# Kernel tuning notes

Hardware: AMD Instinct MI355X
Metric: run time of the kernel (lower is better)

## Reference

```python
import jax, jax.numpy as jnp
import numpy as np

N = 50000      # nodes
E = 800000     # edges per etype
IN, HID, OUT = 128, 128, 64
NH = 4         # heads in layerMH
NE = 2         # interaction edge types
NEG = 0.2      # GATConv leaky_relu negative slope


def _gat(x, src, dst, W, al, ar, b, heads, fdim):
    """DGL GATConv (residual=False, activation=None, bias=True).
    x: (N, in); W: (in, heads*fdim); al/ar: (heads, fdim); b: (heads*fdim,)
    Returns (N, heads, fdim)."""
    n = x.shape[0]
    z = (x @ W).reshape(n, heads, fdim)              # (N,H,F)
    el = jnp.sum(z * al, axis=-1)                    # (N,H)
    er = jnp.sum(z * ar, axis=-1)                    # (N,H)
    e = jax.nn.leaky_relu(el[src] + er[dst], NEG)    # (E,H)
    # edge softmax over incoming edges of each dst node
    m = jax.ops.segment_max(e, dst, num_segments=n)
    m = jnp.where(jnp.isfinite(m), m, 0.0)           # zero in-degree safety
    ex = jnp.exp(e - m[dst])
    den = jax.ops.segment_sum(ex, dst, num_segments=n)
    alpha = ex / jnp.maximum(den[dst], 1e-9)         # (E,H)
    out = jax.ops.segment_sum(alpha[:, :, None] * z[src], dst, num_segments=n)
    return out + b.reshape(1, heads, fdim)


def setup_inputs() -> dict:
    key = jax.random.key(0)
    ks = jax.random.split(key, 19)
    x = jax.random.normal(ks[0], (N, IN), jnp.float32)
    src0 = jax.random.randint(ks[1], (E,), 0, N, jnp.int32)
    dst0 = jax.random.randint(ks[2], (E,), 0, N, jnp.int32)
    src1 = jax.random.randint(ks[3], (E,), 0, N, jnp.int32)
    dst1 = jax.random.randint(ks[4], (E,), 0, N, jnp.int32)
    # per-etype GAT params (stacked over the NE edge types)
    W1 = jax.random.normal(ks[5], (NE, IN, HID), jnp.float32) / np.sqrt(IN)
    a_l1 = jax.random.normal(ks[6], (NE, 1, HID), jnp.float32) * 0.1
    a_r1 = jax.random.normal(ks[7], (NE, 1, HID), jnp.float32) * 0.1
    b1 = jnp.zeros((NE, HID), jnp.float32)
    W2 = jax.random.normal(ks[8], (NE, HID, OUT), jnp.float32) / np.sqrt(HID)
    a_l2 = jax.random.normal(ks[9], (NE, 1, OUT), jnp.float32) * 0.1
    a_r2 = jax.random.normal(ks[10], (NE, 1, OUT), jnp.float32) * 0.1
    b2 = jnp.zeros((NE, OUT), jnp.float32)
    Wm = jax.random.normal(ks[11], (NE, OUT, NH * OUT), jnp.float32) / np.sqrt(OUT)
    a_lm = jax.random.normal(ks[12], (NE, NH, OUT), jnp.float32) * 0.1
    a_rm = jax.random.normal(ks[13], (NE, NH, OUT), jnp.float32) * 0.1
    bm = jnp.zeros((NE, NH * OUT), jnp.float32)
    fc_w = jax.random.normal(ks[14], (NE, NE), jnp.float32) * (np.sqrt(2.0) / np.sqrt(NE))
    return dict(x=x, src0=src0, dst0=dst0, src1=src1, dst1=dst1,
                W1=W1, a_l1=a_l1, a_r1=a_r1, b1=b1,
                W2=W2, a_l2=a_l2, a_r2=a_r2, b2=b2,
                Wm=Wm, a_lm=a_lm, a_rm=a_rm, bm=bm, fc_w=fc_w)


def reference(x, src0, dst0, src1, dst1, W1, a_l1, a_r1, b1,
              W2, a_l2, a_r2, b2, Wm, a_lm, a_rm, bm, fc_w):
    srcs, dsts = (src0, src1), (dst0, dst1)
    # layer1: HeteroGraphConv mean over edge types, single head -> (N, HID)
    h1 = jnp.mean(jnp.stack([
        _gat(x, srcs[i], dsts[i], W1[i], a_l1[i], a_r1[i], b1[i], 1, HID)[:, 0, :]
        for i in range(NE)]), axis=0)
    # layer2: agg_func = fc over stacked etype axis, then mean -> (N, OUT)
    h2s = jnp.stack([
        _gat(h1, srcs[i], dsts[i], W2[i], a_l2[i], a_r2[i], b2[i], 1, OUT)[:, 0, :]
        for i in range(NE)], axis=-1)                       # (N, OUT, NE)
    h2 = jnp.mean(jnp.einsum('noe,fe->nof', h2s, fc_w), axis=-1)
    # multi-head layer: mean over edge types -> (N, NH, OUT)
    hm = jnp.mean(jnp.stack([
        _gat(h2, srcs[i], dsts[i], Wm[i], a_lm[i], a_rm[i], bm[i], NH, OUT)
        for i in range(NE)]), axis=0)
    # per-head mean-centering over nodes (vectorized over heads)
    return hm - jnp.mean(hm, axis=0, keepdims=True)
```

## Files before the change

### kernel.cpp

```cpp
#include <hip/hip_runtime.h>

#define NN 50000
#define EE 800000

using short8v = __attribute__((ext_vector_type(8))) short;
using f32x4 = __attribute__((ext_vector_type(4))) float;

__device__ inline unsigned int bf_pack(float lo, float hi) {
  unsigned int a = __float_as_uint(lo);
  a += 0x7FFFu + ((a >> 16) & 1u);
  unsigned int b = __float_as_uint(hi);
  b += 0x7FFFu + ((b >> 16) & 1u);
  return (a >> 16) | ((b >> 16) << 16);
}
__device__ inline void bf_dec8(uint4 v, float* f) {
  f[0] = __uint_as_float(v.x << 16); f[1] = __uint_as_float(v.x & 0xFFFF0000u);
  f[2] = __uint_as_float(v.y << 16); f[3] = __uint_as_float(v.y & 0xFFFF0000u);
  f[4] = __uint_as_float(v.z << 16); f[5] = __uint_as_float(v.z & 0xFFFF0000u);
  f[6] = __uint_as_float(v.w << 16); f[7] = __uint_as_float(v.w & 0xFFFF0000u);
}
__device__ inline float lrelu(float v) { return v >= 0.f ? v : 0.2f * v; }

__device__ inline void split_pack8(const float* v, uint4& h, uint4& l) {
  unsigned int hb[8], lb[8];
  #pragma unroll
  for (int j = 0; j < 8; j++) {
    unsigned int b = __float_as_uint(v[j]);
    hb[j] = b & 0xFFFF0000u;
    float r = v[j] - __uint_as_float(hb[j]);
    lb[j] = __float_as_uint(r) & 0xFFFF0000u;
  }
  h.x = (hb[0] >> 16) | hb[1]; h.y = (hb[2] >> 16) | hb[3];
  h.z = (hb[4] >> 16) | hb[5]; h.w = (hb[6] >> 16) | hb[7];
  l.x = (lb[0] >> 16) | lb[1]; l.y = (lb[2] >> 16) | lb[3];
  l.z = (lb[4] >> 16) | lb[5]; l.w = (lb[6] >> 16) | lb[7];
}

#define SC_BPR 256

__global__ __launch_bounds__(256) void deg2_k(
    const int* __restrict__ dst0, const int* __restrict__ dst1,
    int* __restrict__ deg) {
  int i = blockIdx.x * 256 + threadIdx.x;
  if (i < 200000) {
    int4 d = ((const int4*)dst0)[i];
    atomicAdd(&deg[d.x], 1); atomicAdd(&deg[d.y], 1);
    atomicAdd(&deg[d.z], 1); atomicAdd(&deg[d.w], 1);
  } else if (i < 400000) {
    int4 d = ((const int4*)dst1)[i - 200000];
    int* dg = deg + 50000;
    atomicAdd(&dg[d.x], 1); atomicAdd(&dg[d.y], 1);
    atomicAdd(&dg[d.z], 1); atomicAdd(&dg[d.w], 1);
  }
}

__global__ __launch_bounds__(512) void scan1_k(const int* __restrict__ deg,
                                               int* __restrict__ inc,
                                               int* __restrict__ bsum) {
  __shared__ int s[512];
  int e = blockIdx.y;
  int t = threadIdx.x, i = blockIdx.x * 512 + t;
  int v = (i < NN) ? deg[e * 50000 + i] : 0;
  s[t] = v; __syncthreads();
  #pragma unroll
  for (int off = 1; off < 512; off <<= 1) {
    int u = (t >= off) ? s[t - off] : 0;
    __syncthreads();
    s[t] += u;
    __syncthreads();
  }
  if (i < NN) inc[e * 50000 + i] = s[t];
  if (t == 511) bsum[e * 128 + blockIdx.x] = s[511];
}

__global__ __launch_bounds__(128) void scan2_k(int* __restrict__ bsum, int nb) {
  __shared__ int s[128];
  int e = blockIdx.x;
  int t = threadIdx.x;
  int v = (t < nb) ? bsum[e * 128 + t] : 0;
  s[t] = v; __syncthreads();
  #pragma unroll
  for (int off = 1; off < 128; off <<= 1) {
    int u = (t >= off) ? s[t - off] : 0;
    __syncthreads();
    s[t] += u;
    __syncthreads();
  }
  if (t < nb) bsum[e * 128 + t] = s[t] - v;
}

__global__ __launch_bounds__(256) void scan3_k(const int* __restrict__ deg,
                                               const int* __restrict__ inc,
                                               const int* __restrict__ bsum,
                                               int* __restrict__ rowptr,
                                               int* __restrict__ cursor) {
  int e = blockIdx.y;
  int i = blockIdx.x * 256 + threadIdx.x;
  if (i < NN) {
    int v = inc[e * 50000 + i] - deg[e * 50000 + i] + bsum[e * 128 + (i >> 9)];
    rowptr[e * 50001 + i] = v;
    cursor[e * 50000 + i] = v;
  }
  if (i == NN) rowptr[e * 50001 + NN] = EE;
}

__global__ __launch_bounds__(256) void csr_scatter2_k(
    const int* __restrict__ src0, const int* __restrict__ dst0,
    const int* __restrict__ src1, const int* __restrict__ dst1,
    int* __restrict__ cursor, int* __restrict__ csr_src) {
  const int range = blockIdx.x & 7;
  const int bpr = blockIdx.x >> 3;
  const int lo = range * 6250;
  const int hi = lo + 6250;
  #pragma unroll
  for (int e = 0; e < 2; e++) {
    const int4* ds4 = (const int4*)(e ? dst1 : dst0);
    const int* ss = e ? src1 : src0;
    int* cur = cursor + e * 50000;
    int* outp = csr_src + (size_t)e * EE;
    for (int i = bpr * 256 + threadIdx.x; i < EE / 4; i += SC_BPR * 256) {
      int4 d = ds4[i];
      int b = i * 4;
      if (d.x >= lo && d.x < hi) {
        int pos = atomicAdd(&cur[d.x], 1);
        outp[pos] = ss[b];
      }
      if (d.y >= lo && d.y < hi) {
        int pos = atomicAdd(&cur[d.y], 1);
        outp[pos] = ss[b + 1];
      }
      if (d.z >= lo && d.z < hi) {
        int pos = atomicAdd(&cur[d.z], 1);
        outp[pos] = ss[b + 2];
      }
      if (d.w >= lo && d.w < hi) {
        int pos = atomicAdd(&cur[d.w], 1);
        outp[pos] = ss[b + 3];
      }
    }
  }
}

__global__ __launch_bounds__(256) void fold_k(
    const float* __restrict__ W1, const float* __restrict__ al1, const float* __restrict__ ar1,
    const float* __restrict__ W2, const float* __restrict__ al2, const float* __restrict__ ar2,
    const float* __restrict__ Wm, const float* __restrict__ alm, const float* __restrict__ arm,
    float* __restrict__ wl1, float* __restrict__ wr1,
    float* __restrict__ wl2, float* __restrict__ wr2,
    float* __restrict__ wlm, float* __restrict__ wrm) {
  int t = blockIdx.x * 256 + threadIdx.x;
  if (t < 512) {
    int lr = t >> 8, e = (t >> 7) & 1, k = t & 127;
    const float* a = (lr ? ar1 : al1) + e * 128;
    const float* w = W1 + ((size_t)e * 128 + k) * 128;
    float s = 0.f;
    for (int f = 0; f < 128; f++) s += w[f] * a[f];
    (lr ? wr1 : wl1)[e * 128 + k] = s;
  } else if (t < 1024) {
    int u = t - 512;
    int lr = u >> 8, e = (u >> 7) & 1, k = u & 127;
    const float* a = (lr ? ar2 : al2) + e * 64;
    const float* w = W2 + ((size_t)e * 128 + k) * 64;
    float s = 0.f;
    for (int f = 0; f < 64; f++) s += w[f] * a[f];
    (lr ? wr2 : wl2)[e * 128 + k] = s;
  } else if (t < 2048) {
    int u = t - 1024;
    int lr = u >> 9, e = (u >> 8) & 1, h = (u >> 6) & 3, k = u & 63;
    const float* a = (lr ? arm : alm) + (e * 4 + h) * 64;
    const float* w = Wm + ((size_t)e * 64 + k) * 256 + h * 64;
    float s = 0.f;
    for (int f = 0; f < 64; f++) s += w[f] * a[f];
    (lr ? wrm : wlm)[(e * 4 + h) * 64 + k] = s;
  }
}

__global__ __launch_bounds__(256) void wtrans_k(
    const float* __restrict__ W1, const float* __restrict__ W2,
    const float* __restrict__ Wm,
    unsigned short* __restrict__ w1h, unsigned short* __restrict__ w1l,
    unsigned short* __restrict__ w2h, unsigned short* __restrict__ w2l,
    unsigned short* __restrict__ wmh, unsigned short* __restrict__ wml) {
  int t = blockIdx.x * 256 + threadIdx.x;
  float v; unsigned short *ph, *pl; int oi;
  if (t < 32768) {
    int j = t & 7, n = (t >> 3) & 127, kg = (t >> 10) & 15, e = t >> 14;
    v = W1[((size_t)(e * 128 + kg * 8 + j)) * 128 + n];
    ph = w1h; pl = w1l; oi = t;
  } else if (t < 49152) {
    int i = t - 32768;
    int j = i & 7, n = (i >> 3) & 63, kg = (i >> 9) & 15, e = i >> 13;
    v = W2[((size_t)(e * 128 + kg * 8 + j)) * 64 + n];
    ph = w2h; pl = w2l; oi = i;
  } else if (t < 81920) {
    int i = t - 49152;
    int j = i & 7, n = (i >> 3) & 255, kg = (i >> 11) & 7, e = i >> 14;
    v = Wm[((size_t)(e * 64 + kg * 8 + j)) * 256 + n];
    ph = wmh; pl = wml; oi = i;
  } else return;
  unsigned int b = __float_as_uint(v);
  unsigned int hb = b & 0xFFFF0000u;
  float r = v - __uint_as_float(hb);
  unsigned int lb = __float_as_uint(r);
  ph[oi] = (unsigned short)(hb >> 16);
  pl[oi] = (unsigned short)(lb >> 16);
}

__global__ __launch_bounds__(256) void xdot_k(
    const float* __restrict__ x, const float* __restrict__ wl,
    const float* __restrict__ wr, unsigned int* __restrict__ xb,
    float* __restrict__ el, float* __restrict__ er) {
  int n = blockIdx.x * 16 + (threadIdx.x >> 4);
  int lane = threadIdx.x & 15;
  if (n >= NN) return;
  float p[4] = {0.f, 0.f, 0.f, 0.f};
  #pragma unroll
  for (int i = 0; i < 2; i++) {
    int c = (lane + i * 16) * 4;
    float4 xv = *(const float4*)(x + (size_t)n * 128 + c);
    uint2 o;
    o.x = bf_pack(xv.x, xv.y);
    o.y = bf_pack(xv.z, xv.w);
    *(uint2*)(xb + (size_t)n * 64 + c / 2) = o;
    #pragma unroll
    for (int e = 0; e < 2; e++) {
      float4 a = *(const float4*)(wl + e * 128 + c);
      float4 b = *(const float4*)(wr + e * 128 + c);
      p[e*2+0] += xv.x*a.x + xv.y*a.y + xv.z*a.z + xv.w*a.w;
      p[e*2+1] += xv.x*b.x + xv.y*b.y + xv.z*b.z + xv.w*b.w;
    }
  }
  #pragma unroll
  for (int off = 1; off < 16; off <<= 1) {
    #pragma unroll
    for (int i = 0; i < 4; i++) p[i] += __shfl_xor(p[i], off);
  }
  if (lane == 0) {
    el[n] = p[0]; er[n] = p[1];
    el[NN + n] = p[2]; er[NN + n] = p[3];
  }
}

__global__ __launch_bounds__(256) void agg_x_f(
    const int* __restrict__ rowptr, const int* __restrict__ csr_src,
    const float* __restrict__ el, const float* __restrict__ er,
    const uint4* __restrict__ xb, float* __restrict__ u1) {
  int d = blockIdx.x * 16 + (threadIdx.x >> 4);
  int lane = threadIdx.x & 15;
  if (d >= NN) return;
  const int e = blockIdx.y;
  const int* rp = rowptr + e * 50001;
  const int* cs = csr_src + (size_t)e * EE;
  const float* elp = el + (size_t)e * NN;
  float erd = er[(size_t)e * NN + d];
  int j0 = rp[d], j1 = rp[d + 1];
  float sm = 0.f;
  float acc[8] = {};
  for (int j = j0; j < j1; j += 16) {
    int cnt = j1 - j; if (cnt > 16) cnt = 16;
    int jj = j + (lane < cnt ? lane : 0);
    int sl = cs[jj];
    float alv = (lane < cnt) ? __expf(lrelu(elp[sl] + erd)) : 0.f;
    sm += alv;
    {
      int sv[8]; float av[8]; uint4 xv[8];
      #pragma unroll
      for (int k = 0; k < 8; k++) {
        sv[k] = __shfl(sl, k, 16);
        av[k] = __shfl(alv, k, 16);
      }
      #pragma unroll
      for (int k = 0; k < 8; k++) xv[k] = xb[(size_t)sv[k] * 16 + lane];
      #pragma unroll
      for (int k = 0; k < 8; k++) {
        float f[8]; bf_dec8(xv[k], f);
        #pragma unroll
        for (int c = 0; c < 8; c++) acc[c] += av[k] * f[c];
      }
    }
    if (cnt > 8) {
      int sv[8]; float av[8]; uint4 xv[8];
      #pragma unroll
      for (int k = 0; k < 8; k++) {
        sv[k] = __shfl(sl, 8 + k, 16);
        av[k] = __shfl(alv, 8 + k, 16);
      }
      #pragma unroll
      for (int k = 0; k < 8; k++) xv[k] = xb[(size_t)sv[k] * 16 + lane];
      #pragma unroll
      for (int k = 0; k < 8; k++) {
        float f[8]; bf_dec8(xv[k], f);
        #pragma unroll
        for (int c = 0; c < 8; c++) acc[c] += av[k] * f[c];
      }
    }
  }
  #pragma unroll
  for (int off = 1; off < 16; off <<= 1) sm += __shfl_xor(sm, off, 16);
  float inv = 1.f / fmaxf(sm, 1e-9f);
  float* up = u1 + ((size_t)e * NN + d) * 128 + lane * 8;
  *(float4*)up       = make_float4(acc[0]*inv, acc[1]*inv, acc[2]*inv, acc[3]*inv);
  *(float4*)(up + 4) = make_float4(acc[4]*inv, acc[5]*inv, acc[6]*inv, acc[7]*inv);
}

__global__ __launch_bounds__(256) void layer12_k(
    const float* __restrict__ u1, const unsigned short* __restrict__ w1h,
    const unsigned short* __restrict__ w1l, const float* __restrict__ b1,
    const unsigned short* __restrict__ w2h, const unsigned short* __restrict__ w2l,
    const float* __restrict__ wl2, const float* __restrict__ wr2,
    unsigned int* __restrict__ Zb, float* __restrict__ el,
    float* __restrict__ er) {
  __shared__ float smem[64 * 132];
  uint4* AsH = (uint4*)smem;
  uint4* AsL = AsH + 256;
  float* Hs = smem;
  const int tid = threadIdx.x;
  const int row0 = blockIdx.x * 64;
  const int wv = tid >> 6, lane = tid & 63;
  const int l15 = lane & 15, lg = lane >> 4;
  const uint4* b1h4 = (const uint4*)w1h;
  const uint4* b1l4 = (const uint4*)w1l;
  const uint4* b2h4 = (const uint4*)w2h;
  const uint4* b2l4 = (const uint4*)w2l;

  f32x4 acc[8] = {};
  for (int e = 0; e < 2; e++) {
    const float* Ap = u1 + (size_t)e * NN * 128;
    for (int k0 = 0; k0 < 128; k0 += 32) {
      {
        int r = tid & 63, kgl = tid >> 6;
        int rr = row0 + r; if (rr >= NN) rr = NN - 1;
        const float* ap = Ap + (size_t)rr * 128 + k0 + kgl * 8;
        float4 a0 = *(const float4*)ap;
        float4 a1 = *(const float4*)(ap + 4);
        float v[8] = {a0.x, a0.y, a0.z, a0.w, a1.x, a1.y, a1.z, a1.w};
        uint4 hh, ll;
        split_pack8(v, hh, ll);
        AsH[kgl * 64 + r] = hh;
        AsL[kgl * 64 + r] = ll;
      }
      __syncthreads();
      int slot = lg * 64 + wv * 16 + l15;
      short8v ah = *reinterpret_cast<const short8v*>(&AsH[slot]);
      short8v al = *reinterpret_cast<const short8v*>(&AsL[slot]);
      int kgb = e * 16 + (k0 >> 3) + lg;
      #pragma unroll
      for (int nf = 0; nf < 8; nf++) {
        int bslot = kgb * 128 + nf * 16 + l15;
        short8v bh = *reinterpret_cast<const short8v*>(&b1h4[bslot]);
        short8v bl = *reinterpret_cast<const short8v*>(&b1l4[bslot]);
        acc[nf] = __builtin_amdgcn_mfma_f32_16x16x32_bf16(ah, bh, acc[nf], 0, 0, 0);
        acc[nf] = __builtin_amdgcn_mfma_f32_16x16x32_bf16(al, bh, acc[nf], 0, 0, 0);
        acc[nf] = __builtin_amdgcn_mfma_f32_16x16x32_bf16(ah, bl, acc[nf], 0, 0, 0);
      }
      __syncthreads();
    }
  }
  #pragma unroll
  for (int nf = 0; nf < 8; nf++) {
    int col = nf * 16 + l15;
    float bb = 0.5f * (b1[col] + b1[128 + col]);
    #pragma unroll
    for (int reg = 0; reg < 4; reg++) {
      int rloc = wv * 16 + lg * 4 + reg;
      Hs[rloc * 132 + col] = 0.5f * acc[nf][reg] + bb;
    }
  }
  __syncthreads();
  {
    int r = tid >> 2, q = tid & 3;
    int grow = row0 + r;
    const float* hrow = Hs + r * 132;
    float p0 = 0.f, p1 = 0.f, p2 = 0.f, p3 = 0.f;
    #pragma unroll 8
    for (int c = 0; c < 32; c++) {
      int k = q + c * 4;
      float hv = hrow[k];
      p0 += hv * wl2[k];       p1 += hv * wr2[k];
      p2 += hv * wl2[128 + k]; p3 += hv * wr2[128 + k];
    }
    p0 += __shfl_xor(p0, 1); p0 += __shfl_xor(p0, 2);
    p1 += __shfl_xor(p1, 1); p1 += __shfl_xor(p1, 2);
    p2 += __shfl_xor(p2, 1); p2 += __shfl_xor(p2, 2);
    p3 += __shfl_xor(p3, 1); p3 += __shfl_xor(p3, 2);
    if (q == 0 && grow < NN) {
      el[grow] = p0;      er[grow] = p1;
      el[NN + grow] = p2; er[NN + grow] = p3;
    }
  }
  f32x4 acc2[2][4] = {};
  for (int k0 = 0; k0 < 128; k0 += 32) {
    int ra = wv * 16 + l15;
    const float* hp = Hs + ra * 132 + k0 + lg * 8;
    float4 h0 = *(const float4*)hp;
    float4 h1v = *(const float4*)(hp + 4);
    float v[8] = {h0.x, h0.y, h0.z, h0.w, h1v.x, h1v.y, h1v.z, h1v.w};
    uint4 hh, ll;
    split_pack8(v, hh, ll);
    short8v ah = *reinterpret_cast<const short8v*>(&hh);
    short8v al = *reinterpret_cast<const short8v*>(&ll);
    #pragma unroll
    for (int e = 0; e < 2; e++) {
      int kgb = e * 16 + (k0 >> 3) + lg;
      #pragma unroll
      for (int nf = 0; nf < 4; nf++) {
        int bslot = kgb * 64 + nf * 16 + l15;
        short8v bh = *reinterpret_cast<const short8v*>(&b2h4[bslot]);
        short8v bl = *reinterpret_cast<const short8v*>(&b2l4[bslot]);
        acc2[e][nf] = __builtin_amdgcn_mfma_f32_16x16x32_bf16(ah, bh, acc2[e][nf], 0, 0, 0);
        acc2[e][nf] = __builtin_amdgcn_mfma_f32_16x16x32_bf16(al, bh, acc2[e][nf], 0, 0, 0);
        acc2[e][nf] = __builtin_amdgcn_mfma_f32_16x16x32_bf16(ah, bl, acc2[e][nf], 0, 0, 0);
      }
    }
  }
  #pragma unroll
  for (int e = 0; e < 2; e++) {
    #pragma unroll
    for (int nf = 0; nf < 4; nf++) {
      #pragma unroll
      for (int reg = 0; reg < 4; reg++) {
        float v = acc2[e][nf][reg];
        float nb = __shfl_xor(v, 1);
        int row = row0 + wv * 16 + lg * 4 + reg;
        if (!(lane & 1) && row < NN) {
          Zb[((size_t)e * NN + row) * 32 + nf * 8 + (l15 >> 1)] = bf_pack(v, nb);
        }
      }
    }
  }
}

__global__ __launch_bounds__(256) void agg2_f(
    const int* __restrict__ rowptr, const int* __restrict__ csr_src,
    const float* __restrict__ el, const float* __restrict__ er,
    const uint4* __restrict__ zb, const float* __restrict__ bias,
    const float* __restrict__ fcw, const float* __restrict__ wlm,
    const float* __restrict__ wrm, uint4* __restrict__ h2b,
    float* __restrict__ elm, float* __restrict__ erm) {
  int d = blockIdx.x * 32 + (threadIdx.x >> 3);
  int lane = threadIdx.x & 7;
  if (d >= NN) return;
  int c0 = lane * 8;
  float coef0 = 0.5f * (fcw[0] + fcw[2]);
  float coef1 = 0.5f * (fcw[1] + fcw[3]);
  float hrow[8];
  #pragma unroll
  for (int c = 0; c < 8; c++)
    hrow[c] = coef0 * bias[c0 + c] + coef1 * bias[64 + c0 + c];
  #pragma unroll
  for (int e = 0; e < 2; e++) {
    const int* rp = rowptr + e * 50001;
    const int* cs = csr_src + (size_t)e * EE;
    const float* elp = el + (size_t)e * NN;
    float erd = er[(size_t)e * NN + d];
    const uint4* zp = zb + (size_t)e * NN * 8;
    int j0 = rp[d], j1 = rp[d + 1];
    float sm = 0.f;
    float acc[8] = {};
    for (int j = j0; j < j1; j += 8) {
      int cnt = j1 - j; if (cnt > 8) cnt = 8;
      int jj = j + (lane < cnt ? lane : 0);
      int sl = cs[jj];
      float alv = (lane < cnt) ? __expf(lrelu(elp[sl] + erd)) : 0.f;
      sm += alv;
      int sv[8]; float av[8]; uint4 zv[8];
      #pragma unroll
      for (int k = 0; k < 8; k++) {
        sv[k] = __shfl(sl, k, 8);
        av[k] = __shfl(alv, k, 8);
      }
      #pragma unroll
      for (int k = 0; k < 8; k++) zv[k] = zp[(size_t)sv[k] * 8 + lane];
      #pragma unroll
      for (int k = 0; k < 8; k++) {
        float f[8]; bf_dec8(zv[k], f);
        #pragma unroll
        for (int c = 0; c < 8; c++) acc[c] += av[k] * f[c];
      }
    }
    #pragma unroll
    for (int off = 1; off < 8; off <<= 1) sm += __shfl_xor(sm, off, 8);
    float cinv = (e ? coef1 : coef0) / fmaxf(sm, 1e-9f);
    #pragma unroll
    for (int c = 0; c < 8; c++) hrow[c] += cinv * acc[c];
  }
  uint4 o;
  o.x = bf_pack(hrow[0], hrow[1]); o.y = bf_pack(hrow[2], hrow[3]);
  o.z = bf_pack(hrow[4], hrow[5]); o.w = bf_pack(hrow[6], hrow[7]);
  h2b[(size_t)d * 8 + lane] = o;
  float p[16];
  #pragma unroll
  for (int e2 = 0; e2 < 2; e2++) {
    #pragma unroll
    for (int h = 0; h < 4; h++) {
      const float* a = wlm + (e2 * 4 + h) * 64 + c0;
      const float* b = wrm + (e2 * 4 + h) * 64 + c0;
      float sl = 0.f, sr = 0.f;
      #pragma unroll
      for (int c = 0; c < 8; c++) { sl += hrow[c] * a[c]; sr += hrow[c] * b[c]; }
      p[e2*4+h] = sl; p[8+e2*4+h] = sr;
    }
  }
  #pragma unroll
  for (int off = 1; off < 8; off <<= 1) {
    #pragma unroll
    for (int i = 0; i < 16; i++) p[i] += __shfl_xor(p[i], off, 8);
  }
  if (lane == 0) *(float4*)(elm + (size_t)d * 4)        = make_float4(p[0], p[1], p[2], p[3]);
  if (lane == 1) *(float4*)(elm + ((size_t)NN + d) * 4) = make_float4(p[4], p[5], p[6], p[7]);
  if (lane == 2) *(float4*)(erm + (size_t)d * 4)        = make_float4(p[8], p[9], p[10], p[11]);
  if (lane == 3) *(float4*)(erm + ((size_t)NN + d) * 4) = make_float4(p[12], p[13], p[14], p[15]);
}

__global__ __launch_bounds__(256) void agg_mh_k(
    const int* __restrict__ rowptr, const int* __restrict__ csr_src,
    const float* __restrict__ elm, const float* __restrict__ erm,
    const uint4* __restrict__ h2b, float* __restrict__ u) {
  int d = blockIdx.x * 32 + (threadIdx.x >> 3);
  int lane = threadIdx.x & 7, c0 = lane * 8;
  if (d >= NN) return;
  const int e = blockIdx.y;
  const int* rp = rowptr + e * 50001;
  const int* cs = csr_src + (size_t)e * EE;
  const float* elp = elm + (size_t)e * NN * 4;
  float4 er4 = *(const float4*)(erm + ((size_t)e * NN + d) * 4);
  int j0 = rp[d], j1 = rp[d + 1];
  float4 sm = make_float4(0.f, 0.f, 0.f, 0.f);
  float acc[4][8] = {};
  for (int j = j0; j < j1; j += 4) {
    int cnt = j1 - j; if (cnt > 4) cnt = 4;
    int sq[4];
    #pragma unroll
    for (int q = 0; q < 4; q++) sq[q] = cs[j + (q < cnt ? q : 0)];
    float4 vq[4]; uint4 hq[4];
    #pragma unroll
    for (int q = 0; q < 4; q++) vq[q] = *(const float4*)(elp + (size_t)sq[q] * 4);
    #pragma unroll
    for (int q = 0; q < 4; q++) hq[q] = h2b[(size_t)sq[q] * 8 + lane];
    #pragma unroll
    for (int q = 0; q < 4; q++) {
      float g = (q < cnt) ? 1.f : 0.f;
      float4 w;
      w.x = g * __expf(lrelu(vq[q].x + er4.x));
      w.y = g * __expf(lrelu(vq[q].y + er4.y));
      w.z = g * __expf(lrelu(vq[q].z + er4.z));
      w.w = g * __expf(lrelu(vq[q].w + er4.w));
      sm.x += w.x; sm.y += w.y; sm.z += w.z; sm.w += w.w;
      float f[8]; bf_dec8(hq[q], f);
      #pragma unroll
      for (int c = 0; c < 8; c++) {
        acc[0][c] += w.x * f[c];
        acc[1][c] += w.y * f[c];
        acc[2][c] += w.z * f[c];
        acc[3][c] += w.w * f[c];
      }
    }
  }
  float4 inv = make_float4(1.f / fmaxf(sm.x, 1e-9f), 1.f / fmaxf(sm.y, 1e-9f),
                           1.f / fmaxf(sm.z, 1e-9f), 1.f / fmaxf(sm.w, 1e-9f));
  float iv[4] = {inv.x, inv.y, inv.z, inv.w};
  #pragma unroll
  for (int h = 0; h < 4; h++) {
    float* up = u + (((size_t)(e * 4 + h) * NN) + d) * 64 + c0;
    *(float4*)up       = make_float4(acc[h][0]*iv[h], acc[h][1]*iv[h],
                                     acc[h][2]*iv[h], acc[h][3]*iv[h]);
    *(float4*)(up + 4) = make_float4(acc[h][4]*iv[h], acc[h][5]*iv[h],
                                     acc[h][6]*iv[h], acc[h][7]*iv[h]);
  }
}

__global__ __launch_bounds__(256) void colsum_u_k(
    const float* __restrict__ u, float* __restrict__ usum) {
  __shared__ float lds[4][64];
  int eh = blockIdx.x >> 6;
  int chunk = blockIdx.x & 63;
  int c = threadIdx.x & 63, rg = threadIdx.x >> 6;
  const float* up = u + (size_t)eh * NN * 64;
  int n0 = chunk * 782;
  int n1 = n0 + 782; if (n1 > NN) n1 = NN;
  float s = 0.f;
  for (int n = n0 + rg; n < n1; n += 4) s += up[(size_t)n * 64 + c];
  lds[rg][c] = s;
  __syncthreads();
  if (rg == 0) {
    float t = lds[0][c] + lds[1][c] + lds[2][c] + lds[3][c];
    unsafeAtomicAdd(&usum[eh * 64 + c], t);
  }
}

__global__ __launch_bounds__(256) void mean_k(
    const float* __restrict__ usum, const float* __restrict__ Wm,
    float* __restrict__ mean) {
  int c = threadIdx.x;
  int h = c >> 6;
  float s = 0.f;
  for (int e = 0; e < 2; e++) {
    const float* us = usum + (e * 4 + h) * 64;
    const float* wp = Wm + (size_t)e * 64 * 256 + c;
    for (int k = 0; k < 64; k++) s += us[k] * wp[(size_t)k * 256];
  }
  mean[c] = s * (0.5f / NN);
}

__global__ __launch_bounds__(256) void out_gemm_k(
    const float* __restrict__ u, const unsigned short* __restrict__ wmh,
    const unsigned short* __restrict__ wml, const float* __restrict__ mean,
    float* __restrict__ out) {
  __shared__ uint4 AsH[512], AsL[512];
  const int h = blockIdx.y;
  const int tid = threadIdx.x;
  const int row0 = blockIdx.x * 128;
  const int wv = tid >> 6, lane = tid & 63;
  const int l15 = lane & 15, lg = lane >> 4;
  f32x4 acc[2][4] = {};
  const uint4* bh4 = (const uint4*)wmh;
  const uint4* bl4 = (const uint4*)wml;
  for (int e = 0; e < 2; e++) {
    const float* Ap = u + (size_t)(e * 4 + h) * NN * 64;
    for (int k0 = 0; k0 < 64; k0 += 32) {
      {
        int r = tid & 127, half = tid >> 7;
        int rr = row0 + r; if (rr >= NN) rr = NN - 1;
        const float* ap = Ap + (size_t)rr * 64 + k0;
        #pragma unroll
        for (int i = 0; i < 2; i++) {
          int kg = half * 2 + i;
          float4 a0 = *(const float4*)(ap + kg * 8);
          float4 a1 = *(const float4*)(ap + kg * 8 + 4);
          float v[8] = {a0.x, a0.y, a0.z, a0.w, a1.x, a1.y, a1.z, a1.w};
          uint4 hh, ll;
          split_pack8(v, hh, ll);
          AsH[kg * 128 + r] = hh;
          AsL[kg * 128 + r] = ll;
        }
      }
      __syncthreads();
      short8v ah[2], al[2];
      #pragma unroll
      for (int mf = 0; mf < 2; mf++) {
        int slot = lg * 128 + wv * 32 + mf * 16 + l15;
        ah[mf] = *reinterpret_cast<const short8v*>(&AsH[slot]);
        al[mf] = *reinterpret_cast<const short8v*>(&AsL[slot]);
      }
      int kgb = e * 8 + (k0 >> 3) + lg;
      #pragma unroll
      for (int nf = 0; nf < 4; nf++) {
        int bslot = kgb * 256 + h * 64 + nf * 16 + l15;
        short8v bh = *reinterpret_cast<const short8v*>(&bh4[bslot]);
        short8v bl = *reinterpret_cast<const short8v*>(&bl4[bslot]);
        #pragma unroll
        for (int mf = 0; mf < 2; mf++) {
          acc[mf][nf] = __builtin_amdgcn_mfma_f32_16x16x32_bf16(ah[mf], bh, acc[mf][nf], 0, 0, 0);
          acc[mf][nf] = __builtin_amdgcn_mfma_f32_16x16x32_bf16(al[mf], bh, acc[mf][nf], 0, 0, 0);
          acc[mf][nf] = __builtin_amdgcn_mfma_f32_16x16x32_bf16(ah[mf], bl, acc[mf][nf], 0, 0, 0);
        }
      }
      __syncthreads();
    }
  }
  #pragma unroll
  for (int nf = 0; nf < 4; nf++) {
    int col = nf * 16 + l15;
    float mn = mean[h * 64 + col];
    #pragma unroll
    for (int mf = 0; mf < 2; mf++) {
      #pragma unroll
      for (int reg = 0; reg < 4; reg++) {
        int row = row0 + wv * 32 + mf * 16 + lg * 4 + reg;
        if (row < NN)
          out[(size_t)row * 256 + h * 64 + col] = 0.5f * acc[mf][nf][reg] - mn;
      }
    }
  }
}

extern "C" void kernel_launch(void* const* d_in, const int* in_sizes, int n_in,
                              void* d_out, int out_size, void* d_ws, size_t ws_size,
                              hipStream_t stream) {
  const float* x  = (const float*)d_in[0];
  const int* src0 = (const int*)d_in[1];
  const int* dst0 = (const int*)d_in[2];
  const int* src1 = (const int*)d_in[3];
  const int* dst1 = (const int*)d_in[4];
  const float* W1  = (const float*)d_in[5];
  const float* al1 = (const float*)d_in[6];
  const float* ar1 = (const float*)d_in[7];
  const float* b1  = (const float*)d_in[8];
  const float* W2  = (const float*)d_in[9];
  const float* al2 = (const float*)d_in[10];
  const float* ar2 = (const float*)d_in[11];
  const float* b2  = (const float*)d_in[12];
  const float* Wm  = (const float*)d_in[13];
  const float* alm = (const float*)d_in[14];
  const float* arm = (const float*)d_in[15];
  const float* fcw = (const float*)d_in[17];
  float* out = (float*)d_out;

  float* ws = (float*)d_ws;
  float* zu     = ws;
  unsigned int* z2b = (unsigned int*)(ws + 12800000);
  unsigned int* xb = (unsigned int*)(ws + 25600000);
  unsigned int* h2b = (unsigned int*)(ws + 32000000);
  float* el     = ws + 33600000;
  float* er     = ws + 34000000;
  float* elm    = ws + 34400000;
  float* erm    = ws + 34800000;
  float* wl1    = ws + 35200000;
  float* wr1    = wl1 + 256;
  float* wl2    = wr1 + 256;
  float* wr2    = wl2 + 256;
  float* wlm    = wr2 + 256;
  float* wrm    = wlm + 512;
  float* usum   = wrm + 512;
  float* meanp  = usum + 512;
  int* rowptr  = (int*)(meanp + 256);
  int* csr_src = rowptr + 100002;
  unsigned short* w1h = (unsigned short*)(csr_src + 2 * EE + 2);
  unsigned short* w1l = w1h + 32768;
  unsigned short* w2h = w1l + 32768;
  unsigned short* w2l = w2h + 16384;
  unsigned short* wmh = w2l + 16384;
  unsigned short* wml = wmh + 32768;
  int* deg    = (int*)el;
  int* inc    = (int*)er;
  int* cursor = (int*)zu;
  int* bsum   = (int*)zu + 200000;

  hipMemsetAsync(deg, 0, 2 * 50000 * sizeof(int), stream);
  hipMemsetAsync(usum, 0, 512 * sizeof(float), stream);
  deg2_k<<<1563, 256, 0, stream>>>(dst0, dst1, deg);
  scan1_k<<<dim3(98, 2), 512, 0, stream>>>(deg, inc, bsum);
  scan2_k<<<2, 128, 0, stream>>>(bsum, 98);
  scan3_k<<<dim3(196, 2), 256, 0, stream>>>(deg, inc, bsum, rowptr, cursor);
  csr_scatter2_k<<<8 * SC_BPR, 256, 0, stream>>>(src0, dst0, src1, dst1,
                                                 cursor, csr_src);

  fold_k<<<8, 256, 0, stream>>>(W1, al1, ar1, W2, al2, ar2, Wm, alm, arm,
                                wl1, wr1, wl2, wr2, wlm, wrm);
  wtrans_k<<<320, 256, 0, stream>>>(W1, W2, Wm, w1h, w1l, w2h, w2l, wmh, wml);

  xdot_k<<<3125, 256, 0, stream>>>(x, wl1, wr1, xb, el, er);
  agg_x_f<<<dim3(3125, 2), 256, 0, stream>>>(rowptr, csr_src, el, er,
                                             (const uint4*)xb, zu);
  layer12_k<<<782, 256, 0, stream>>>(zu, w1h, w1l, b1, w2h, w2l, wl2, wr2,
                                     z2b, el, er);

  agg2_f<<<1563, 256, 0, stream>>>(rowptr, csr_src, el, er, (const uint4*)z2b,
                                   b2, fcw, wlm, wrm, (uint4*)h2b, elm, erm);

  agg_mh_k<<<dim3(1563, 2), 256, 0, stream>>>(rowptr, csr_src, elm, erm,
                                              (const uint4*)h2b, zu);
  colsum_u_k<<<512, 256, 0, stream>>>(zu, usum);
  mean_k<<<1, 256, 0, stream>>>(usum, Wm, meanp);
  out_gemm_k<<<dim3(391, 4), 256, 0, stream>>>(zu, wmh, wml, meanp, out);
}
```

Before: 569.9 us.

## Record per-edge slot during degree count to drop scatter atomics

New measurement: 533.2 us. 6.4% less time.

```diff
diff --git a/kernel.cpp b/kernel.cpp
--- a/kernel.cpp
+++ b/kernel.cpp
@@ -38,19 +38,27 @@
 
 #define SC_BPR 256
 
-__global__ __launch_bounds__(256) void deg2_k(
+__global__ __launch_bounds__(256) void passA_k(
     const int* __restrict__ dst0, const int* __restrict__ dst1,
-    int* __restrict__ deg) {
+    int* __restrict__ deg, int* __restrict__ rel) {
   int i = blockIdx.x * 256 + threadIdx.x;
   if (i < 200000) {
     int4 d = ((const int4*)dst0)[i];
-    atomicAdd(&deg[d.x], 1); atomicAdd(&deg[d.y], 1);
-    atomicAdd(&deg[d.z], 1); atomicAdd(&deg[d.w], 1);
+    int4 r;
+    r.x = atomicAdd(&deg[d.x], 1);
+    r.y = atomicAdd(&deg[d.y], 1);
+    r.z = atomicAdd(&deg[d.z], 1);
+    r.w = atomicAdd(&deg[d.w], 1);
+    ((int4*)rel)[i] = r;
   } else if (i < 400000) {
     int4 d = ((const int4*)dst1)[i - 200000];
     int* dg = deg + 50000;
-    atomicAdd(&dg[d.x], 1); atomicAdd(&dg[d.y], 1);
-    atomicAdd(&dg[d.z], 1); atomicAdd(&dg[d.w], 1);
+    int4 r;
+    r.x = atomicAdd(&dg[d.x], 1);
+    r.y = atomicAdd(&dg[d.y], 1);
+    r.z = atomicAdd(&dg[d.z], 1);
+    r.w = atomicAdd(&dg[d.w], 1);
+    ((int4*)(rel + EE))[i - 200000] = r;
   }
 }
 
@@ -92,51 +100,46 @@
 __global__ __launch_bounds__(256) void scan3_k(const int* __restrict__ deg,
                                                const int* __restrict__ inc,
                                                const int* __restrict__ bsum,
-                                               int* __restrict__ rowptr,
-                                               int* __restrict__ cursor) {
+                                               int* __restrict__ rowptr) {
   int e = blockIdx.y;
   int i = blockIdx.x * 256 + threadIdx.x;
   if (i < NN) {
-    int v = inc[e * 50000 + i] - deg[e * 50000 + i] + bsum[e * 128 + (i >> 9)];
-    rowptr[e * 50001 + i] = v;
-    cursor[e * 50000 + i] = v;
+    rowptr[e * 50001 + i] =
+        inc[e * 50000 + i] - deg[e * 50000 + i] + bsum[e * 128 + (i >> 9)];
   }
   if (i == NN) rowptr[e * 50001 + NN] = EE;
 }
 
-__global__ __launch_bounds__(256) void csr_scatter2_k(
+__global__ __launch_bounds__(256) void passB_k(
     const int* __restrict__ src0, const int* __restrict__ dst0,
     const int* __restrict__ src1, const int* __restrict__ dst1,
-    int* __restrict__ cursor, int* __restrict__ csr_src) {
+    const int* __restrict__ rel, const int* __restrict__ rowptr,
+    int* __restrict__ csr_src) {
+  __shared__ int rp_s[2][6250];
   const int range = blockIdx.x & 7;
   const int bpr = blockIdx.x >> 3;
   const int lo = range * 6250;
   const int hi = lo + 6250;
+  for (int k = threadIdx.x; k < 6250; k += 256) {
+    rp_s[0][k] = rowptr[lo + k];
+    rp_s[1][k] = rowptr[50001 + lo + k];
+  }
+  __syncthreads();
   #pragma unroll
   for (int e = 0; e < 2; e++) {
     const int4* ds4 = (const int4*)(e ? dst1 : dst0);
     const int* ss = e ? src1 : src0;
-    int* cur = cursor + e * 50000;
+    const int4* rl4 = (const int4*)(rel + (size_t)e * EE);
+    const int* rps = rp_s[e];
     int* outp = csr_src + (size_t)e * EE;
     for (int i = bpr * 256 + threadIdx.x; i < EE / 4; i += SC_BPR * 256) {
       int4 d = ds4[i];
+      int4 rl = rl4[i];
       int b = i * 4;
-      if (d.x >= lo && d.x < hi) {
-        int pos = atomicAdd(&cur[d.x], 1);
-        outp[pos] = ss[b];
-      }
-      if (d.y >= lo && d.y < hi) {
-        int pos = atomicAdd(&cur[d.y], 1);
-        outp[pos] = ss[b + 1];
-      }
-      if (d.z >= lo && d.z < hi) {
-        int pos = atomicAdd(&cur[d.z], 1);
-        outp[pos] = ss[b + 2];
-      }
-      if (d.w >= lo && d.w < hi) {
-        int pos = atomicAdd(&cur[d.w], 1);
-        outp[pos] = ss[b + 3];
-      }
+      if (d.x >= lo && d.x < hi) outp[rps[d.x - lo] + rl.x] = ss[b];
+      if (d.y >= lo && d.y < hi) outp[rps[d.y - lo] + rl.y] = ss[b + 1];
+      if (d.z >= lo && d.z < hi) outp[rps[d.z - lo] + rl.z] = ss[b + 2];
+      if (d.w >= lo && d.w < hi) outp[rps[d.w - lo] + rl.w] = ss[b + 3];
     }
   }
 }
@@ -721,19 +724,19 @@
   unsigned short* w2l = w2h + 16384;
   unsigned short* wmh = w2l + 16384;
   unsigned short* wml = wmh + 32768;
+  int* rel    = (int*)zu;
+  int* bsum   = (int*)zu + 2 * EE;
   int* deg    = (int*)el;
   int* inc    = (int*)er;
-  int* cursor = (int*)zu;
-  int* bsum   = (int*)zu + 200000;
 
   hipMemsetAsync(deg, 0, 2 * 50000 * sizeof(int), stream);
   hipMemsetAsync(usum, 0, 512 * sizeof(float), stream);
-  deg2_k<<<1563, 256, 0, stream>>>(dst0, dst1, deg);
+  passA_k<<<1563, 256, 0, stream>>>(dst0, dst1, deg, rel);
   scan1_k<<<dim3(98, 2), 512, 0, stream>>>(deg, inc, bsum);
   scan2_k<<<2, 128, 0, stream>>>(bsum, 98);
-  scan3_k<<<dim3(196, 2), 256, 0, stream>>>(deg, inc, bsum, rowptr, cursor);
-  csr_scatter2_k<<<8 * SC_BPR, 256, 0, stream>>>(src0, dst0, src1, dst1,
-                                                 cursor, csr_src);
+  scan3_k<<<dim3(196, 2), 256, 0, stream>>>(deg, inc, bsum, rowptr);
+  passB_k<<<8 * SC_BPR, 256, 0, stream>>>(src0, dst0, src1, dst1,
+                                          rel, rowptr, csr_src);
 
   fold_k<<<8, 256, 0, stream>>>(W1, al1, ar1, W2, al2, ar2, Wm, alm, arm,
                                 wl1, wr1, wl2, wr2, wlm, wrm);
```
